# Performance work log

Hardware: AMD Instinct MI355X
Metric: run time of the kernel (lower is better)

The kernel has to match this reference:

```python
import jax, jax.numpy as jnp
import numpy as np

B, C, L = 4, 512, 2048
H, D = 8, C // 8  # n_heads, attention_size


def conv1d_same(x, w, b):
    # x: [B, C, L], w: [Cout, Cin, 3], b: [Cout]; padding='same'
    y = jax.lax.conv_general_dilated(x, w, window_strides=(1,), padding='SAME',
                                     dimension_numbers=('NCH', 'OIH', 'NCH'))
    return y + b[None, :, None]


def setup_inputs() -> dict:
    key = jax.random.key(0)
    ks = jax.random.split(key, 11)
    s = 0.02
    inp = {
        'q': jax.random.normal(ks[0], (B, C, L), jnp.float32),
        'k': jax.random.normal(ks[1], (B, C, L), jnp.float32),
        'v': jax.random.normal(ks[2], (B, C, L), jnp.float32),
        'wq_w': jax.random.normal(ks[3], (C, C, 3), jnp.float32) * s,
        'wq_b': jnp.zeros((C,), jnp.float32),
        'wk_w': jax.random.normal(ks[4], (C, C, 3), jnp.float32) * s,
        'wk_b': jnp.zeros((C,), jnp.float32),
        'wv_w': jax.random.normal(ks[5], (C, C, 3), jnp.float32) * s,
        'wv_b': jnp.zeros((C,), jnp.float32),
        'fc_w': jax.random.normal(ks[6], (C, C, 3), jnp.float32) * s,
        'fc_b': jnp.zeros((C,), jnp.float32),
    }
    return inp


def reference(q, k, v, wq_w, wq_b, wk_w, wk_b, wv_w, wv_b, fc_w, fc_b):
    b = q.shape[0]
    # Faithful to torch: conv output [B,C,L] is row-major reshaped to [B,L,H,D]
    qh = conv1d_same(q, wq_w, wq_b).reshape(b, -1, H, D).transpose(0, 2, 1, 3)  # [B,H,L,D]
    kh = conv1d_same(k, wk_w, wk_b).reshape(b, -1, H, D).transpose(0, 2, 3, 1)  # [B,H,D,L]
    vh = conv1d_same(v, wv_w, wv_b).reshape(b, -1, H, D).transpose(0, 2, 1, 3)  # [B,H,L,D]
    # NOTE: original divides by attention_size D, not sqrt(D)
    attn = jax.nn.softmax(jnp.matmul(qh, kh) / D, axis=-1)  # [B,H,L,L]
    out = jnp.matmul(attn, vh)                               # [B,H,L,D]
    out = out.transpose(0, 2, 1, 3).reshape(b, H * D, -1)    # [B,C,L]
    return conv1d_same(out, fc_w, fc_b)
```

## Files before the change

### kernel.cpp

```cpp
#include <hip/hip_runtime.h>
#include <hip/hip_bf16.h>

#define BB 4
#define NH 8
#define HD 64
#define CC 512
#define LL 2048
#define KK 1536
#define LPAD 2050

#define QS 0.022542110013890054f

typedef float f32x4 __attribute__((ext_vector_type(4)));
typedef short bf16x8 __attribute__((ext_vector_type(8)));

static __device__ __forceinline__ ushort f2bf(float f) {
  union { float f; unsigned u; } v; v.f = f;
  unsigned r = v.u + 0x7fffu + ((v.u >> 16) & 1u);
  return (ushort)(r >> 16);
}
static __device__ __forceinline__ void gload16(const ushort* g, ushort* l) {
  __builtin_amdgcn_global_load_lds((const __attribute__((address_space(1))) void*)g,
                                   (__attribute__((address_space(3))) void*)l, 16, 0, 0);
}

__global__ void prep_w(const float* __restrict__ w0, const float* __restrict__ w1,
                       const float* __restrict__ w2, const float* __restrict__ w3,
                       ushort* __restrict__ out)
{
  int i = blockIdx.x * 256 + threadIdx.x;
  const int per = CC * KK;
  if (i >= 4 * per) return;
  int cidx = i / per;
  int rem  = i - cidx * per;
  int co   = rem / KK;
  int kk   = rem - co * KK;
  int t = kk >> 9, ci = kk & 511;
  const float* w = (cidx == 0) ? w0 : (cidx == 1) ? w1 : (cidx == 2) ? w2 : w3;
  out[i] = f2bf(w[((size_t)co * CC + ci) * 3 + t]);
}

__device__ __forceinline__ void transpose_body(const float* __restrict__ xb,
                                               ushort* __restrict__ ob)
{
  const int c0 = blockIdx.y * 64;
  const int l0 = blockIdx.x * 64;
  const int tid = threadIdx.x;
  __shared__ ushort T[64 * 72];
  {
    const int rr = tid >> 4;
    const int f4 = tid & 15;
#pragma unroll
    for (int it = 0; it < 4; ++it) {
      const int cc = rr + it * 16;
      ushort s[4];
      float4 vv = *(const float4*)(xb + (size_t)(c0 + cc) * LL + l0 + f4 * 4);
      s[0] = f2bf(vv.x); s[1] = f2bf(vv.y); s[2] = f2bf(vv.z); s[3] = f2bf(vv.w);
      *(ushort4*)&T[cc * 72 + f4 * 4] = *(ushort4*)s;
    }
  }
  __syncthreads();
  {
    const int lr = tid >> 3;
    const int ch = tid & 7;
#pragma unroll
    for (int it = 0; it < 2; ++it) {
      const int ll = lr + it * 32;
      ushort tmp[8];
#pragma unroll
      for (int e = 0; e < 8; ++e) tmp[e] = T[(ch * 8 + e) * 72 + ll];
      *(uint4*)(ob + (size_t)(l0 + ll + 1) * CC + c0 + ch * 8) = *(uint4*)tmp;
    }
  }
  if (blockIdx.x == 0 && tid < 8) {
    uint4 z4 = make_uint4(0, 0, 0, 0);
    *(uint4*)(ob + c0 + tid * 8) = z4;
  }
  if (blockIdx.x == (LL / 64 - 1) && tid >= 248) {
    uint4 z4 = make_uint4(0, 0, 0, 0);
    *(uint4*)(ob + (size_t)(LPAD - 1) * CC + c0 + (tid - 248) * 8) = z4;
  }
}

__global__ __launch_bounds__(256, 4)
void transpose_k(const float* __restrict__ in, ushort* __restrict__ outT)
{
  const int b = blockIdx.z;
  transpose_body(in + (size_t)b * CC * LL, outT + (size_t)b * (LPAD * CC));
}

__global__ __launch_bounds__(256, 4)
void transpose3_k(const float* __restrict__ q, const float* __restrict__ k,
                  const float* __restrict__ v, ushort* __restrict__ xq,
                  ushort* __restrict__ xk, ushort* __restrict__ xv)
{
  const int z = blockIdx.z;
  const int b = z & 3, var = z >> 2;
  const float* in = (var == 0) ? q : (var == 1) ? k : v;
  ushort* out = (var == 0) ? xq : (var == 1) ? xk : xv;
  transpose_body(in + (size_t)b * CC * LL, out + (size_t)b * (LPAD * CC));
}

template<int BM>
__device__ __forceinline__ void conv_body(const ushort* __restrict__ xb,
                                          const ushort* __restrict__ Wt,
                                          const float* __restrict__ bias,
                                          void* __restrict__ outp, int mode, int b,
                                          float scale)
{
  const int co0 = blockIdx.y * BM;
  const int l0  = blockIdx.x * 128;
  const int tid = threadIdx.x;
  const int lane = tid & 63;
  const int w    = tid >> 6;
  const int col  = lane & 15, quad = lane >> 4;
  constexpr int MI = BM / 32;

  __shared__ ushort Asl[BM * 64];
  __shared__ ushort Bsl[128 * 64];

  const int sr = tid >> 3;
  const int g8 = ((tid & 7) ^ (sr & 7)) * 8;
  const ushort* ag  = Wt + (size_t)(co0 + sr) * KK + g8;
  const ushort* bg  = xb + (size_t)(l0 + sr) * CC + g8;
  ushort* alds = &Asl[tid * 8];
  ushort* blds = &Bsl[tid * 8];

  f32x4 acc[MI][4] = {};
  const int wm = (w & 1) * (BM / 2);
  const int wn = (w >> 1) * 64;
  const int c7 = col & 7;

  for (int k0 = 0; k0 < KK; k0 += 64) {
#pragma unroll
    for (int r2 = 0; r2 < MI; ++r2)
      gload16(ag + (size_t)(r2 * 32) * KK + k0, alds + r2 * 2048);
#pragma unroll
    for (int r2 = 0; r2 < 4; ++r2)
      gload16(bg + (size_t)(r2 * 32) * CC + k0, blds + r2 * 2048);
    __syncthreads();
#pragma unroll
    for (int kk = 0; kk < 2; ++kk) {
      bf16x8 af[MI], bfr[4];
#pragma unroll
      for (int i = 0; i < MI; ++i)
        af[i] = *(const bf16x8*)&Asl[(wm + i * 16 + col) * 64 + (((kk * 4 + quad) ^ c7) * 8)];
#pragma unroll
      for (int j = 0; j < 4; ++j)
        bfr[j] = *(const bf16x8*)&Bsl[(wn + j * 16 + col) * 64 + (((kk * 4 + quad) ^ c7) * 8)];
#pragma unroll
      for (int i = 0; i < MI; ++i)
#pragma unroll
        for (int j = 0; j < 4; ++j)
          acc[i][j] = __builtin_amdgcn_mfma_f32_16x16x32_bf16(af[i], bfr[j], acc[i][j], 0, 0, 0);
    }
    __syncthreads();
  }

#pragma unroll
  for (int i = 0; i < MI; ++i) {
#pragma unroll
    for (int r = 0; r < 4; ++r) {
      const int co = co0 + wm + i * 16 + quad * 4 + r;
      const float bi = bias[co];
#pragma unroll
      for (int j = 0; j < 4; ++j) {
        const int l = l0 + wn + j * 16 + col;
        const float y = (acc[i][j][r] + bi) * scale;
        if (mode == 0) {
          const int xx = (co << 2) + (l >> 9);
          const int hh = (l >> 6) & 7;
          const int dd = l & 63;
          ((ushort*)outp)[((size_t)(b * NH + hh) * LL + xx) * HD + dd] = f2bf(y);
        } else if (mode == 1) {
          const int xx = (co << 2) + (l >> 9);
          const int hh = (l >> 6) & 7;
          const int dd = l & 63;
          ((ushort*)outp)[((size_t)(b * NH + hh) * HD + dd) * LL + xx] = f2bf(y);
        } else {
          ((float*)outp)[(size_t)(b * CC + co) * LL + l] = y;
        }
      }
    }
  }
}

template<int BM>
__global__ __launch_bounds__(256, 3)
void conv_k(const ushort* __restrict__ xT, const ushort* __restrict__ Wt,
            const float* __restrict__ bias, void* __restrict__ outp, int mode,
            float scale)
{
  const int b = blockIdx.z;
  conv_body<BM>(xT + (size_t)b * (LPAD * CC), Wt, bias, outp, mode, b, scale);
}

__global__ __launch_bounds__(256, 3)
void conv3_k(const ushort* __restrict__ xq, const ushort* __restrict__ xk,
             const ushort* __restrict__ xv, const ushort* __restrict__ Wt,
             const float* __restrict__ b0, const float* __restrict__ b1,
             const float* __restrict__ b2, ushort* __restrict__ o0,
             ushort* __restrict__ o1, ushort* __restrict__ o2)
{
  const int z = blockIdx.z;
  const int b = z & 3, var = z >> 2;
  const ushort* xT = (var == 0) ? xq : (var == 1) ? xk : xv;
  const float* bias = (var == 0) ? b0 : (var == 1) ? b1 : b2;
  ushort* outp = (var == 0) ? o0 : (var == 1) ? o1 : o2;
  const float scale = (var == 0) ? QS : 1.0f;
  conv_body<128>(xT + (size_t)b * (LPAD * CC), Wt + (size_t)var * CC * KK, bias, outp,
                 (var == 2) ? 1 : 0, b, scale);
}

__global__ __launch_bounds__(512, 4)
void attn_k(const ushort* __restrict__ qh, const ushort* __restrict__ kh,
            const ushort* __restrict__ vt, ushort* __restrict__ obT)
{
  const int id   = blockIdx.x;
  const int xcd  = id & 7;
  const int slot = id >> 3;
  const int bh   = xcd * 4 + (slot >> 4);
  const int x0   = (slot & 15) * 128;
  const int b = bh >> 3, h = bh & 7;
  const int tid = threadIdx.x, lane = tid & 63, wv = tid >> 6;
  const int col = lane & 15, quad = lane >> 4;
  const int wx = wv * 16;
  const int c7 = col & 7;

  __shared__ ushort Kv[2][8192];
  __shared__ ushort Ps[128 * 88];

  const ushort* Qg = qh + (size_t)bh * (LL * HD);
  const ushort* Kg = kh + (size_t)bh * (LL * HD);
  const ushort* Vg = vt + (size_t)bh * (HD * LL);
  ushort* ob = obT + (size_t)b * (LPAD * CC);

  const int sr = tid >> 3;
  const int g8 = ((tid & 7) ^ (sr & 7)) * 8;

  bf16x8 aq[2];
#pragma unroll
  for (int kk = 0; kk < 2; ++kk)
    aq[kk] = *(const bf16x8*)(Qg + (size_t)(x0 + wx + col) * HD + kk * 32 + quad * 8);

  const short one = (short)0x3F80;
  const bf16x8 ones = {one, one, one, one, one, one, one, one};

  f32x4 oacc[4] = {};
  f32x4 dacc = {};

  {
    gload16(Kg + (size_t)sr * HD + g8, &Kv[0][tid * 8]);
    gload16(Vg + (size_t)sr * LL + g8, &Kv[0][4096 + tid * 8]);
  }

  for (int yt = 0; yt < 32; ++yt) {
    const int cur = yt & 1;
    __syncthreads();
    if (yt + 1 < 32) {
      const int y1 = (yt + 1) * 64;
      gload16(Kg + (size_t)(y1 + sr) * HD + g8, &Kv[1 - cur][tid * 8]);
      gload16(Vg + (size_t)sr * LL + y1 + g8, &Kv[1 - cur][4096 + tid * 8]);
    }
    const ushort* Kb = &Kv[cur][0];
    const ushort* Vb = &Kv[cur][4096];

    f32x4 sacc[4] = {};
#pragma unroll
    for (int kk = 0; kk < 2; ++kk)
#pragma unroll
      for (int j = 0; j < 4; ++j) {
        bf16x8 bk = *(const bf16x8*)&Kb[(j * 16 + col) * 64 + (((kk * 4 + quad) ^ c7) * 8)];
        sacc[j] = __builtin_amdgcn_mfma_f32_16x16x32_bf16(bk, aq[kk], sacc[j], 0, 0, 0);
      }
#pragma unroll
    for (int j = 0; j < 4; ++j) {
      union { __hip_bfloat162 h[2]; uint2 u; } pk;
      pk.h[0] = __float22bfloat162_rn(make_float2(__builtin_amdgcn_exp2f(sacc[j][0]),
                                                 __builtin_amdgcn_exp2f(sacc[j][1])));
      pk.h[1] = __float22bfloat162_rn(make_float2(__builtin_amdgcn_exp2f(sacc[j][2]),
                                                 __builtin_amdgcn_exp2f(sacc[j][3])));
      *(uint2*)&Ps[(wx + col) * 88 + j * 16 + quad * 4] = pk.u;
    }
#pragma unroll
    for (int kk = 0; kk < 2; ++kk) {
      bf16x8 ap = *(const bf16x8*)&Ps[(wx + col) * 88 + kk * 32 + quad * 8];
      dacc = __builtin_amdgcn_mfma_f32_16x16x32_bf16(ap, ones, dacc, 0, 0, 0);
#pragma unroll
      for (int j = 0; j < 4; ++j) {
        bf16x8 bv = *(const bf16x8*)&Vb[(j * 16 + col) * 64 + (((kk * 4 + quad) ^ c7) * 8)];
        oacc[j] = __builtin_amdgcn_mfma_f32_16x16x32_bf16(ap, bv, oacc[j], 0, 0, 0);
      }
    }
  }

#pragma unroll
  for (int r = 0; r < 4; ++r) {
    const int xg = x0 + wx + quad * 4 + r;
    const float inv = 1.f / dacc[r];
#pragma unroll
    for (int j = 0; j < 4; ++j) {
      const int d = j * 16 + col;
      const int flat = xg * 512 + h * 64 + d;
      const int c = flat >> 11, l = flat & 2047;
      ob[(size_t)(l + 1) * CC + c] = f2bf(oacc[j][r] * inv);
    }
  }
  if ((slot & 15) == 0 && tid < 128) {
    const int rw = tid >> 6;
    const int cc = h * 64 + (tid & 63);
    ob[(size_t)(rw ? (LPAD - 1) : 0) * CC + cc] = 0;
  }
}

extern "C" void kernel_launch(void* const* d_in, const int* in_sizes, int n_in,
                              void* d_out, int out_size, void* d_ws, size_t ws_size,
                              hipStream_t stream) {
  const float* q    = (const float*)d_in[0];
  const float* k    = (const float*)d_in[1];
  const float* v    = (const float*)d_in[2];
  const float* wq_w = (const float*)d_in[3];
  const float* wq_b = (const float*)d_in[4];
  const float* wk_w = (const float*)d_in[5];
  const float* wk_b = (const float*)d_in[6];
  const float* wv_w = (const float*)d_in[7];
  const float* wv_b = (const float*)d_in[8];
  const float* fc_w = (const float*)d_in[9];
  const float* fc_b = (const float*)d_in[10];

  char* ws = (char*)d_ws;
  const size_t WSZ = (size_t)CC * KK * sizeof(ushort);
  const size_t HSZ = (size_t)BB * NH * LL * HD * sizeof(ushort);
  const size_t XSZ = (size_t)BB * LPAD * CC * sizeof(ushort);
  const size_t FUSED_NEED = 4 * WSZ + 3 * HSZ + 3 * XSZ;

  ushort* Wt = (ushort*)(ws);
  prep_w<<<(4 * CC * KK + 255) / 256, 256, 0, stream>>>(wq_w, wk_w, wv_w, fc_w, Wt);

  if (ws_size >= FUSED_NEED) {
    ushort* qh  = (ushort*)(ws + 4 * WSZ);
    ushort* kh  = (ushort*)(ws + 4 * WSZ + HSZ);
    ushort* vt  = (ushort*)(ws + 4 * WSZ + 2 * HSZ);
    ushort* xTq = (ushort*)(ws + 4 * WSZ + 3 * HSZ);
    ushort* xTk = (ushort*)(ws + 4 * WSZ + 3 * HSZ + XSZ);
    ushort* xTv = (ushort*)(ws + 4 * WSZ + 3 * HSZ + 2 * XSZ);
    ushort* obT = xTq;

    transpose3_k<<<dim3(32, 8, 12), 256, 0, stream>>>(q, k, v, xTq, xTk, xTv);
    conv3_k<<<dim3(16, 4, 12), 256, 0, stream>>>(xTq, xTk, xTv, Wt,
                                                 wq_b, wk_b, wv_b, qh, kh, vt);
    attn_k<<<512, 512, 0, stream>>>(qh, kh, vt, obT);
    conv_k<64><<<dim3(16, 8, 4), 256, 0, stream>>>(obT, Wt + 3 * CC * KK, fc_b,
                                                   (float*)d_out, 2, 1.0f);
  } else {
    ushort* qh  = (ushort*)(ws + 4 * WSZ);
    ushort* kh  = (ushort*)(ws + 4 * WSZ + HSZ);
    ushort* vt  = (ushort*)(ws + 4 * WSZ + 2 * HSZ);
    ushort* xTb = (ushort*)(ws + 4 * WSZ + 3 * HSZ);
    ushort* obT = xTb;

    transpose_k<<<dim3(32, 8, 4), 256, 0, stream>>>(q, xTb);
    conv_k<128><<<dim3(16, 4, 4), 256, 0, stream>>>(xTb, Wt + 0 * CC * KK, wq_b, qh, 0, QS);
    transpose_k<<<dim3(32, 8, 4), 256, 0, stream>>>(k, xTb);
    conv_k<128><<<dim3(16, 4, 4), 256, 0, stream>>>(xTb, Wt + 1 * CC * KK, wk_b, kh, 0, 1.0f);
    transpose_k<<<dim3(32, 8, 4), 256, 0, stream>>>(v, xTb);
    conv_k<128><<<dim3(16, 4, 4), 256, 0, stream>>>(xTb, Wt + 2 * CC * KK, wv_b, vt, 1, 1.0f);
    attn_k<<<512, 512, 0, stream>>>(qh, kh, vt, obT);
    conv_k<64><<<dim3(16, 8, 4), 256, 0, stream>>>(obT, Wt + 3 * CC * KK, fc_b,
                                                   (float*)d_out, 2, 1.0f);
  }
}
```

Before: 256.8 us.

## Load K/V fragments directly from global memory instead of LDS double buffer

```diff
diff --git a/kernel.cpp b/kernel.cpp
--- a/kernel.cpp
+++ b/kernel.cpp
@@ -225,9 +225,7 @@
   const int tid = threadIdx.x, lane = tid & 63, wv = tid >> 6;
   const int col = lane & 15, quad = lane >> 4;
   const int wx = wv * 16;
-  const int c7 = col & 7;
-
-  __shared__ ushort Kv[2][8192];
+
   __shared__ ushort Ps[128 * 88];
 
   const ushort* Qg = qh + (size_t)bh * (LL * HD);
@@ -235,44 +233,46 @@
   const ushort* Vg = vt + (size_t)bh * (HD * LL);
   ushort* ob = obT + (size_t)b * (LPAD * CC);
 
-  const int sr = tid >> 3;
-  const int g8 = ((tid & 7) ^ (sr & 7)) * 8;
-
   bf16x8 aq[2];
 #pragma unroll
   for (int kk = 0; kk < 2; ++kk)
     aq[kk] = *(const bf16x8*)(Qg + (size_t)(x0 + wx + col) * HD + kk * 32 + quad * 8);
 
+  const ushort* Kf = Kg + (size_t)col * HD + quad * 8;
+  const ushort* Vf = Vg + (size_t)col * LL + quad * 8;
+
   const short one = (short)0x3F80;
   const bf16x8 ones = {one, one, one, one, one, one, one, one};
 
   f32x4 oacc[4] = {};
   f32x4 dacc = {};
 
-  {
-    gload16(Kg + (size_t)sr * HD + g8, &Kv[0][tid * 8]);
-    gload16(Vg + (size_t)sr * LL + g8, &Kv[0][4096 + tid * 8]);
-  }
-
   for (int yt = 0; yt < 32; ++yt) {
-    const int cur = yt & 1;
-    __syncthreads();
-    if (yt + 1 < 32) {
-      const int y1 = (yt + 1) * 64;
-      gload16(Kg + (size_t)(y1 + sr) * HD + g8, &Kv[1 - cur][tid * 8]);
-      gload16(Vg + (size_t)sr * LL + y1 + g8, &Kv[1 - cur][4096 + tid * 8]);
-    }
-    const ushort* Kb = &Kv[cur][0];
-    const ushort* Vb = &Kv[cur][4096];
-
+    const int ybase = yt * 64;
+
+    bf16x8 kf[4][2];
+#pragma unroll
+    for (int j = 0; j < 4; ++j)
+#pragma unroll
+      for (int kk = 0; kk < 2; ++kk)
+        kf[j][kk] = *(const bf16x8*)(Kf + (size_t)(ybase + j * 16) * HD + kk * 32);
+
+    __builtin_amdgcn_s_setprio(1);
     f32x4 sacc[4] = {};
 #pragma unroll
     for (int kk = 0; kk < 2; ++kk)
 #pragma unroll
-      for (int j = 0; j < 4; ++j) {
-        bf16x8 bk = *(const bf16x8*)&Kb[(j * 16 + col) * 64 + (((kk * 4 + quad) ^ c7) * 8)];
-        sacc[j] = __builtin_amdgcn_mfma_f32_16x16x32_bf16(bk, aq[kk], sacc[j], 0, 0, 0);
-      }
+      for (int j = 0; j < 4; ++j)
+        sacc[j] = __builtin_amdgcn_mfma_f32_16x16x32_bf16(kf[j][kk], aq[kk], sacc[j], 0, 0, 0);
+    __builtin_amdgcn_s_setprio(0);
+
+    bf16x8 vf[4][2];
+#pragma unroll
+    for (int j = 0; j < 4; ++j)
+#pragma unroll
+      for (int kk = 0; kk < 2; ++kk)
+        vf[j][kk] = *(const bf16x8*)(Vf + (size_t)j * (16 * LL) + ybase + kk * 32);
+
 #pragma unroll
     for (int j = 0; j < 4; ++j) {
       union { __hip_bfloat162 h[2]; uint2 u; } pk;
@@ -282,15 +282,16 @@
                                                  __builtin_amdgcn_exp2f(sacc[j][3])));
       *(uint2*)&Ps[(wx + col) * 88 + j * 16 + quad * 4] = pk.u;
     }
+
 #pragma unroll
     for (int kk = 0; kk < 2; ++kk) {
       bf16x8 ap = *(const bf16x8*)&Ps[(wx + col) * 88 + kk * 32 + quad * 8];
+      __builtin_amdgcn_s_setprio(1);
       dacc = __builtin_amdgcn_mfma_f32_16x16x32_bf16(ap, ones, dacc, 0, 0, 0);
 #pragma unroll
-      for (int j = 0; j < 4; ++j) {
-        bf16x8 bv = *(const bf16x8*)&Vb[(j * 16 + col) * 64 + (((kk * 4 + quad) ^ c7) * 8)];
-        oacc[j] = __builtin_amdgcn_mfma_f32_16x16x32_bf16(ap, bv, oacc[j], 0, 0, 0);
-      }
+      for (int j = 0; j < 4; ++j)
+        oacc[j] = __builtin_amdgcn_mfma_f32_16x16x32_bf16(ap, vf[j][kk], oacc[j], 0, 0, 0);
+      __builtin_amdgcn_s_setprio(0);
     }
   }
 
```

Result: slower. 436.0 us (+69.7%).

## Switch attention kernel to 32x32x16 MFMA tiles with four waves per block

Applied to the files above, without the earlier changes.

```diff
diff --git a/kernel.cpp b/kernel.cpp
--- a/kernel.cpp
+++ b/kernel.cpp
@@ -12,6 +12,7 @@
 #define QS 0.022542110013890054f
 
 typedef float f32x4 __attribute__((ext_vector_type(4)));
+typedef float f32x16 __attribute__((ext_vector_type(16)));
 typedef short bf16x8 __attribute__((ext_vector_type(8)));
 
 static __device__ __forceinline__ ushort f2bf(float f) {
@@ -212,7 +213,7 @@
                  (var == 2) ? 1 : 0, b, scale);
 }
 
-__global__ __launch_bounds__(512, 4)
+__global__ __launch_bounds__(256, 2)
 void attn_k(const ushort* __restrict__ qh, const ushort* __restrict__ kh,
             const ushort* __restrict__ vt, ushort* __restrict__ obT)
 {
@@ -223,12 +224,11 @@
   const int x0   = (slot & 15) * 128;
   const int b = bh >> 3, h = bh & 7;
   const int tid = threadIdx.x, lane = tid & 63, wv = tid >> 6;
-  const int col = lane & 15, quad = lane >> 4;
-  const int wx = wv * 16;
-  const int c7 = col & 7;
+  const int l31 = lane & 31, hi = lane >> 5, l7 = lane & 7;
+  const int xloc = wv * 32 + l31;
 
   __shared__ ushort Kv[2][8192];
-  __shared__ ushort Ps[128 * 88];
+  __shared__ ushort Ps[128 * 72];
 
   const ushort* Qg = qh + (size_t)bh * (LL * HD);
   const ushort* Kg = kh + (size_t)bh * (LL * HD);
@@ -238,20 +238,23 @@
   const int sr = tid >> 3;
   const int g8 = ((tid & 7) ^ (sr & 7)) * 8;
 
-  bf16x8 aq[2];
-#pragma unroll
-  for (int kk = 0; kk < 2; ++kk)
-    aq[kk] = *(const bf16x8*)(Qg + (size_t)(x0 + wx + col) * HD + kk * 32 + quad * 8);
+  bf16x8 qf[4];
+#pragma unroll
+  for (int ks = 0; ks < 4; ++ks)
+    qf[ks] = *(const bf16x8*)(Qg + (size_t)(x0 + xloc) * HD + ks * 16 + hi * 8);
 
   const short one = (short)0x3F80;
   const bf16x8 ones = {one, one, one, one, one, one, one, one};
 
-  f32x4 oacc[4] = {};
-  f32x4 dacc = {};
+  f32x16 oacc[2] = {};
+  f32x16 dacc = {};
 
   {
-    gload16(Kg + (size_t)sr * HD + g8, &Kv[0][tid * 8]);
-    gload16(Vg + (size_t)sr * LL + g8, &Kv[0][4096 + tid * 8]);
+    ushort* kb = &Kv[0][tid * 8];
+    gload16(Kg + (size_t)sr * HD + g8, kb);
+    gload16(Kg + (size_t)(32 + sr) * HD + g8, kb + 2048);
+    gload16(Vg + (size_t)sr * LL + g8, kb + 4096);
+    gload16(Vg + (size_t)(32 + sr) * LL + g8, kb + 6144);
   }
 
   for (int yt = 0; yt < 32; ++yt) {
@@ -259,51 +262,65 @@
     __syncthreads();
     if (yt + 1 < 32) {
       const int y1 = (yt + 1) * 64;
-      gload16(Kg + (size_t)(y1 + sr) * HD + g8, &Kv[1 - cur][tid * 8]);
-      gload16(Vg + (size_t)sr * LL + y1 + g8, &Kv[1 - cur][4096 + tid * 8]);
+      ushort* kb = &Kv[1 - cur][tid * 8];
+      gload16(Kg + (size_t)(y1 + sr) * HD + g8, kb);
+      gload16(Kg + (size_t)(y1 + 32 + sr) * HD + g8, kb + 2048);
+      gload16(Vg + (size_t)sr * LL + y1 + g8, kb + 4096);
+      gload16(Vg + (size_t)(32 + sr) * LL + y1 + g8, kb + 6144);
     }
     const ushort* Kb = &Kv[cur][0];
     const ushort* Vb = &Kv[cur][4096];
 
-    f32x4 sacc[4] = {};
-#pragma unroll
-    for (int kk = 0; kk < 2; ++kk)
-#pragma unroll
-      for (int j = 0; j < 4; ++j) {
-        bf16x8 bk = *(const bf16x8*)&Kb[(j * 16 + col) * 64 + (((kk * 4 + quad) ^ c7) * 8)];
-        sacc[j] = __builtin_amdgcn_mfma_f32_16x16x32_bf16(bk, aq[kk], sacc[j], 0, 0, 0);
+    f32x16 sacc[2] = {};
+#pragma unroll
+    for (int mt = 0; mt < 2; ++mt) {
+      const int row = mt * 32 + l31;
+#pragma unroll
+      for (int ks = 0; ks < 4; ++ks) {
+        const int ch = (ks * 2 + hi) ^ l7;
+        bf16x8 kf = *(const bf16x8*)&Kb[row * 64 + ch * 8];
+        sacc[mt] = __builtin_amdgcn_mfma_f32_32x32x16_bf16(kf, qf[ks], sacc[mt], 0, 0, 0);
       }
-#pragma unroll
-    for (int j = 0; j < 4; ++j) {
-      union { __hip_bfloat162 h[2]; uint2 u; } pk;
-      pk.h[0] = __float22bfloat162_rn(make_float2(__builtin_amdgcn_exp2f(sacc[j][0]),
-                                                 __builtin_amdgcn_exp2f(sacc[j][1])));
-      pk.h[1] = __float22bfloat162_rn(make_float2(__builtin_amdgcn_exp2f(sacc[j][2]),
-                                                 __builtin_amdgcn_exp2f(sacc[j][3])));
-      *(uint2*)&Ps[(wx + col) * 88 + j * 16 + quad * 4] = pk.u;
-    }
-#pragma unroll
-    for (int kk = 0; kk < 2; ++kk) {
-      bf16x8 ap = *(const bf16x8*)&Ps[(wx + col) * 88 + kk * 32 + quad * 8];
-      dacc = __builtin_amdgcn_mfma_f32_16x16x32_bf16(ap, ones, dacc, 0, 0, 0);
-#pragma unroll
-      for (int j = 0; j < 4; ++j) {
-        bf16x8 bv = *(const bf16x8*)&Vb[(j * 16 + col) * 64 + (((kk * 4 + quad) ^ c7) * 8)];
-        oacc[j] = __builtin_amdgcn_mfma_f32_16x16x32_bf16(ap, bv, oacc[j], 0, 0, 0);
+    }
+
+#pragma unroll
+    for (int mt = 0; mt < 2; ++mt)
+#pragma unroll
+      for (int rq = 0; rq < 4; ++rq) {
+        union { __hip_bfloat162 h2[2]; uint2 u; } pk;
+        pk.h2[0] = __float22bfloat162_rn(make_float2(
+            __builtin_amdgcn_exp2f(sacc[mt][rq * 4 + 0]),
+            __builtin_amdgcn_exp2f(sacc[mt][rq * 4 + 1])));
+        pk.h2[1] = __float22bfloat162_rn(make_float2(
+            __builtin_amdgcn_exp2f(sacc[mt][rq * 4 + 2]),
+            __builtin_amdgcn_exp2f(sacc[mt][rq * 4 + 3])));
+        *(uint2*)&Ps[xloc * 72 + mt * 32 + rq * 8 + hi * 4] = pk.u;
       }
-    }
-  }
-
-#pragma unroll
-  for (int r = 0; r < 4; ++r) {
-    const int xg = x0 + wx + quad * 4 + r;
-    const float inv = 1.f / dacc[r];
-#pragma unroll
-    for (int j = 0; j < 4; ++j) {
-      const int d = j * 16 + col;
+
+#pragma unroll
+    for (int ks = 0; ks < 4; ++ks) {
+      bf16x8 pa = *(const bf16x8*)&Ps[xloc * 72 + ks * 16 + hi * 8];
+      dacc = __builtin_amdgcn_mfma_f32_32x32x16_bf16(pa, ones, dacc, 0, 0, 0);
+#pragma unroll
+      for (int nt = 0; nt < 2; ++nt) {
+        const int rowd = nt * 32 + l31;
+        const int ch = (ks * 2 + hi) ^ l7;
+        bf16x8 vf = *(const bf16x8*)&Vb[rowd * 64 + ch * 8];
+        oacc[nt] = __builtin_amdgcn_mfma_f32_32x32x16_bf16(pa, vf, oacc[nt], 0, 0, 0);
+      }
+    }
+  }
+
+#pragma unroll
+  for (int reg = 0; reg < 16; ++reg) {
+    const int xg = x0 + wv * 32 + (reg & 3) + 8 * (reg >> 2) + 4 * hi;
+    const float inv = 1.f / dacc[reg];
+#pragma unroll
+    for (int nt = 0; nt < 2; ++nt) {
+      const int d = nt * 32 + l31;
       const int flat = xg * 512 + h * 64 + d;
       const int c = flat >> 11, l = flat & 2047;
-      ob[(size_t)(l + 1) * CC + c] = f2bf(oacc[j][r] * inv);
+      ob[(size_t)(l + 1) * CC + c] = f2bf(oacc[nt][reg] * inv);
     }
   }
   if ((slot & 15) == 0 && tid < 128) {
@@ -349,7 +366,7 @@
     transpose3_k<<<dim3(32, 8, 12), 256, 0, stream>>>(q, k, v, xTq, xTk, xTv);
     conv3_k<<<dim3(16, 4, 12), 256, 0, stream>>>(xTq, xTk, xTv, Wt,
                                                  wq_b, wk_b, wv_b, qh, kh, vt);
-    attn_k<<<512, 512, 0, stream>>>(qh, kh, vt, obT);
+    attn_k<<<512, 256, 0, stream>>>(qh, kh, vt, obT);
     conv_k<64><<<dim3(16, 8, 4), 256, 0, stream>>>(obT, Wt + 3 * CC * KK, fc_b,
                                                    (float*)d_out, 2, 1.0f);
   } else {
@@ -365,7 +382,7 @@
     conv_k<128><<<dim3(16, 4, 4), 256, 0, stream>>>(xTb, Wt + 1 * CC * KK, wk_b, kh, 0, 1.0f);
     transpose_k<<<dim3(32, 8, 4), 256, 0, stream>>>(v, xTb);
     conv_k<128><<<dim3(16, 4, 4), 256, 0, stream>>>(xTb, Wt + 2 * CC * KK, wv_b, vt, 1, 1.0f);
-    attn_k<<<512, 512, 0, stream>>>(qh, kh, vt, obT);
+    attn_k<<<512, 256, 0, stream>>>(qh, kh, vt, obT);
     conv_k<64><<<dim3(16, 8, 4), 256, 0, stream>>>(obT, Wt + 3 * CC * KK, fc_b,
                                                    (float*)d_out, 2, 1.0f);
   }
```

Result: no change. 252.2 us (-1.8%).

## Load V fragments directly to registers and unroll attention loop by two

Applied to the files above, without the earlier changes.

```diff
diff --git a/kernel.cpp b/kernel.cpp
--- a/kernel.cpp
+++ b/kernel.cpp
@@ -227,7 +227,7 @@
   const int wx = wv * 16;
   const int c7 = col & 7;
 
-  __shared__ ushort Kv[2][8192];
+  __shared__ ushort Kv[2][4096];
   __shared__ ushort Ps[128 * 88];
 
   const ushort* Qg = qh + (size_t)bh * (LL * HD);
@@ -238,6 +238,8 @@
   const int sr = tid >> 3;
   const int g8 = ((tid & 7) ^ (sr & 7)) * 8;
 
+  const ushort* Vgl = Vg + (size_t)col * LL + quad * 8;
+
   bf16x8 aq[2];
 #pragma unroll
   for (int kk = 0; kk < 2; ++kk)
@@ -249,50 +251,75 @@
   f32x4 oacc[4] = {};
   f32x4 dacc = {};
 
-  {
-    gload16(Kg + (size_t)sr * HD + g8, &Kv[0][tid * 8]);
-    gload16(Vg + (size_t)sr * LL + g8, &Kv[0][4096 + tid * 8]);
-  }
-
-  for (int yt = 0; yt < 32; ++yt) {
-    const int cur = yt & 1;
+  bf16x8 vfA[4][2], vfB[4][2];
+
+#define LOAD_VF(vf, ybase)                                                  \
+  {                                                                         \
+    _Pragma("unroll")                                                       \
+    for (int j = 0; j < 4; ++j) {                                           \
+      const ushort* p = Vgl + (size_t)j * (16 * LL) + (ybase);              \
+      vf[j][0] = *(const bf16x8*)(p);                                       \
+      vf[j][1] = *(const bf16x8*)(p + 32);                                  \
+    }                                                                       \
+  }
+
+#define TILE_COMPUTE(Kb, vf)                                                \
+  {                                                                         \
+    f32x4 sacc[4] = {};                                                     \
+    __builtin_amdgcn_s_setprio(1);                                          \
+    _Pragma("unroll")                                                       \
+    for (int kk = 0; kk < 2; ++kk)                                          \
+      _Pragma("unroll")                                                     \
+      for (int j = 0; j < 4; ++j) {                                         \
+        bf16x8 bk = *(const bf16x8*)&(Kb)[(j * 16 + col) * 64 +             \
+                                          (((kk * 4 + quad) ^ c7) * 8)];    \
+        sacc[j] = __builtin_amdgcn_mfma_f32_16x16x32_bf16(bk, aq[kk],       \
+                                                          sacc[j], 0, 0, 0);\
+      }                                                                     \
+    __builtin_amdgcn_s_setprio(0);                                          \
+    _Pragma("unroll")                                                       \
+    for (int j = 0; j < 4; ++j) {                                           \
+      union { __hip_bfloat162 hh[2]; uint2 u; } pk;                         \
+      pk.hh[0] = __float22bfloat162_rn(                                     \
+          make_float2(__builtin_amdgcn_exp2f(sacc[j][0]),                   \
+                      __builtin_amdgcn_exp2f(sacc[j][1])));                 \
+      pk.hh[1] = __float22bfloat162_rn(                                     \
+          make_float2(__builtin_amdgcn_exp2f(sacc[j][2]),                   \
+                      __builtin_amdgcn_exp2f(sacc[j][3])));                 \
+      *(uint2*)&Ps[(wx + col) * 88 + j * 16 + quad * 4] = pk.u;             \
+    }                                                                       \
+    __builtin_amdgcn_s_setprio(1);                                          \
+    _Pragma("unroll")                                                       \
+    for (int kk = 0; kk < 2; ++kk) {                                        \
+      bf16x8 ap = *(const bf16x8*)&Ps[(wx + col) * 88 + kk * 32 + quad * 8];\
+      dacc = __builtin_amdgcn_mfma_f32_16x16x32_bf16(ap, ones, dacc,        \
+                                                     0, 0, 0);              \
+      _Pragma("unroll")                                                     \
+      for (int j = 0; j < 4; ++j)                                           \
+        oacc[j] = __builtin_amdgcn_mfma_f32_16x16x32_bf16(ap, (vf)[j][kk],  \
+                                                          oacc[j], 0, 0, 0);\
+    }                                                                       \
+    __builtin_amdgcn_s_setprio(0);                                          \
+  }
+
+  gload16(Kg + (size_t)sr * HD + g8, &Kv[0][tid * 8]);
+  LOAD_VF(vfA, 0);
+
+  for (int yt = 0; yt < 32; yt += 2) {
     __syncthreads();
-    if (yt + 1 < 32) {
-      const int y1 = (yt + 1) * 64;
-      gload16(Kg + (size_t)(y1 + sr) * HD + g8, &Kv[1 - cur][tid * 8]);
-      gload16(Vg + (size_t)sr * LL + y1 + g8, &Kv[1 - cur][4096 + tid * 8]);
-    }
-    const ushort* Kb = &Kv[cur][0];
-    const ushort* Vb = &Kv[cur][4096];
-
-    f32x4 sacc[4] = {};
-#pragma unroll
-    for (int kk = 0; kk < 2; ++kk)
-#pragma unroll
-      for (int j = 0; j < 4; ++j) {
-        bf16x8 bk = *(const bf16x8*)&Kb[(j * 16 + col) * 64 + (((kk * 4 + quad) ^ c7) * 8)];
-        sacc[j] = __builtin_amdgcn_mfma_f32_16x16x32_bf16(bk, aq[kk], sacc[j], 0, 0, 0);
-      }
-#pragma unroll
-    for (int j = 0; j < 4; ++j) {
-      union { __hip_bfloat162 h[2]; uint2 u; } pk;
-      pk.h[0] = __float22bfloat162_rn(make_float2(__builtin_amdgcn_exp2f(sacc[j][0]),
-                                                 __builtin_amdgcn_exp2f(sacc[j][1])));
-      pk.h[1] = __float22bfloat162_rn(make_float2(__builtin_amdgcn_exp2f(sacc[j][2]),
-                                                 __builtin_amdgcn_exp2f(sacc[j][3])));
-      *(uint2*)&Ps[(wx + col) * 88 + j * 16 + quad * 4] = pk.u;
-    }
-#pragma unroll
-    for (int kk = 0; kk < 2; ++kk) {
-      bf16x8 ap = *(const bf16x8*)&Ps[(wx + col) * 88 + kk * 32 + quad * 8];
-      dacc = __builtin_amdgcn_mfma_f32_16x16x32_bf16(ap, ones, dacc, 0, 0, 0);
-#pragma unroll
-      for (int j = 0; j < 4; ++j) {
-        bf16x8 bv = *(const bf16x8*)&Vb[(j * 16 + col) * 64 + (((kk * 4 + quad) ^ c7) * 8)];
-        oacc[j] = __builtin_amdgcn_mfma_f32_16x16x32_bf16(ap, bv, oacc[j], 0, 0, 0);
-      }
-    }
-  }
+    gload16(Kg + (size_t)((yt + 1) * 64 + sr) * HD + g8, &Kv[1][tid * 8]);
+    LOAD_VF(vfB, (yt + 1) * 64);
+    TILE_COMPUTE(Kv[0], vfA);
+
+    __syncthreads();
+    if (yt + 2 < 32) {
+      gload16(Kg + (size_t)((yt + 2) * 64 + sr) * HD + g8, &Kv[0][tid * 8]);
+      LOAD_VF(vfA, (yt + 2) * 64);
+    }
+    TILE_COMPUTE(Kv[1], vfB);
+  }
+#undef LOAD_VF
+#undef TILE_COMPUTE
 
 #pragma unroll
   for (int r = 0; r < 4; ++r) {
```

Result: slower. 338.4 us (+31.7%).
